# Optimization experiments

Measured on AMD Instinct MI355X. Metric: run time of the kernel, lower is better.

The kernel has to match this reference:

```python
import jax, jax.numpy as jnp
import numpy as np

B, Q, K, D = 16, 2048, 2048, 128
NEG = -1000000.0  # matches torch module's mask fill value (not -inf)


def setup_inputs() -> dict:
    key = jax.random.key(0)
    kq, kk, kv, kl = jax.random.split(key, 4)
    q = jax.random.normal(kq, (B, Q, D), dtype=jnp.float32)
    k = jax.random.normal(kk, (B, K, D), dtype=jnp.float32)
    v = jax.random.normal(kv, (B, K, D), dtype=jnp.float32)
    valid_lens = jax.random.randint(kl, (B, 1), 0, K, dtype=jnp.int32)
    return {"q": q, "k": k, "v": v, "valid_lens": valid_lens}


def reference(q, k, v, valid_lens):
    d = q.shape[-1]
    # scores: (B, Q, K)
    weight = jnp.einsum('bqd,bkd->bqk', q, k) / jnp.sqrt(jnp.asarray(d, q.dtype))
    # mask: key position j valid iff j < valid_len[b]; broadcast over query dim
    mask = jnp.arange(k.shape[1])[None, None, :] < valid_lens[:, :, None]  # (B,1,K)
    weight = jnp.where(mask, weight, NEG)
    score = jax.nn.softmax(weight, axis=-1)
    return jnp.einsum('bqk,bkv->bqv', score, v)
```

## Files before the change

kernel.cpp:

```cpp
#include <hip/hip_runtime.h>

constexpr int NB = 16;
constexpr int NQ = 2048;
constexpr int NK = 2048;
constexpr int ND = 128;
constexpr int KVBLK = 64;
constexpr int NTILE = NK / KVBLK;
constexpr int TILE_USH = KVBLK * ND;
constexpr float SCALE = 0.08838834764831844f;

typedef __attribute__((ext_vector_type(4))) float f4;
typedef __attribute__((ext_vector_type(16))) float f32x16;
typedef __attribute__((ext_vector_type(8))) unsigned short us8;
typedef __attribute__((ext_vector_type(8))) __bf16 bf16x8;
typedef __attribute__((ext_vector_type(4))) unsigned int u32x4;

static __device__ __forceinline__ unsigned short f2bf(float f) {
    unsigned u = __builtin_bit_cast(unsigned, f);
    u += 0x7fffu + ((u >> 16) & 1u);
    return (unsigned short)(u >> 16);
}
static __device__ __forceinline__ f4 splat4(float x) { f4 r = {x,x,x,x}; return r; }

static __device__ __forceinline__ void load_lds16(const unsigned short* g, unsigned short* l) {
    __builtin_amdgcn_global_load_lds(
        (const __attribute__((address_space(1))) void*)g,
        (__attribute__((address_space(3))) void*)l,
        16, 0, 0);
}

static __device__ __forceinline__ unsigned cvt_pk_bf16(float lo, float hi) {
    unsigned r;
    asm("v_cvt_pk_bf16_f32 %0, %1, %2" : "=v"(r) : "v"(lo), "v"(hi));
    return r;
}

__global__ __launch_bounds__(256)
void prep_kv4(const float* __restrict__ kg, const float* __restrict__ vg,
              unsigned short* __restrict__ wk, unsigned short* __restrict__ wvt)
{
    const int b   = blockIdx.y;
    const int t   = blockIdx.x;
    const int kv0 = t * KVBLK;
    const int t0  = threadIdx.x;

    __shared__ __align__(16) unsigned short vl[64 * 136];

    {
        const int kv = t0 >> 2;
        const int c  = t0 & 3;
        const float* gp = kg + (size_t)(b * NK + kv0 + kv) * ND + c * 32;
        unsigned short* ob = wk + (size_t)(b * NTILE + t) * TILE_USH;
        #pragma unroll
        for (int g = 0; g < 4; ++g) {
            f4 f0 = *(const f4*)(gp + g * 8);
            f4 f1 = *(const f4*)(gp + g * 8 + 4);
            us8 w;
            #pragma unroll
            for (int i = 0; i < 4; ++i) { w[i] = f2bf(f0[i]); w[i+4] = f2bf(f1[i]); }
            const int d0 = c * 32 + g * 8;
            const int f  = (kv >> 5) * 8 + (d0 >> 4);
            const int off = f * 512 + ((d0 >> 3) & 1) * 256 + (kv & 31) * 8;
            *(us8*)(ob + off) = w;
        }
    }
    {
        const int kv = t0 >> 2;
        const int d0 = (t0 & 3) * 32;
        const float* gp = vg + (size_t)(b * NK + kv0 + kv) * ND + d0;
        unsigned short* lb = &vl[kv * 136 + d0];
        #pragma unroll
        for (int g = 0; g < 4; ++g) {
            f4 f0 = *(const f4*)(gp + g * 8);
            f4 f1 = *(const f4*)(gp + g * 8 + 4);
            us8 w;
            #pragma unroll
            for (int i = 0; i < 4; ++i) { w[i] = f2bf(f0[i]); w[i+4] = f2bf(f1[i]); }
            *(us8*)(lb + g * 8) = w;
        }
    }
    __syncthreads();
    {
        unsigned short* ob = wvt + (size_t)(b * NTILE + t) * TILE_USH;
        #pragma unroll
        for (int iter = 0; iter < 4; ++iter) {
            const int cid = iter * 256 + t0;
            const int f   = cid >> 6;
            const int l   = cid & 63;
            const int kb  = (f >> 2) * 16 + (l >> 5) * 8;
            const int d   = (f & 3) * 32 + (l & 31);
            us8 w;
            #pragma unroll
            for (int j = 0; j < 8; ++j) w[j] = vl[(kb + j) * 136 + d];
            *(us8*)(ob + cid * 8) = w;
        }
    }
}

__global__ __launch_bounds__(512, 2)
void attn_fused7(const float* __restrict__ qg, const int* __restrict__ vlen,
                 const unsigned short* __restrict__ wk,
                 const unsigned short* __restrict__ wvt,
                 float* __restrict__ og)
{
    const int bid = blockIdx.x;
    const int b   = bid & 15;
    const int qc  = bid >> 4;
    const int q0  = qc * 128;

    const int tid  = threadIdx.x;
    const int wid  = tid >> 6;
    const int grp  = wid >> 2;
    const int w4   = wid & 3;
    const int lane = tid & 63;
    const int lq   = lane & 31;
    const int hi   = lane >> 5;

    const int L = vlen[b];
    const bool uniform = (L <= 0);
    const int Leff = uniform ? NK : L;
    const int ntiles = (Leff + KVBLK - 1) / KVBLK;
    const int ng    = (ntiles + 1 - grp) >> 1;
    const int niter = (ntiles + 1) >> 1;

    __shared__ __align__(16) unsigned short smem[2][2][2 * TILE_USH];

    bf16x8 aq[8];
    {
        const float* qp = qg + (size_t)(b * NQ + q0 + w4 * 32 + lq) * ND + hi * 8;
        #pragma unroll
        for (int c = 0; c < 8; ++c) {
            f4 f0 = *(const f4*)(qp + c * 16);
            f4 f1 = *(const f4*)(qp + c * 16 + 4);
            us8 u;
            #pragma unroll
            for (int i = 0; i < 4; ++i) {
                u[i]     = f2bf(f0[i] * SCALE);
                u[i + 4] = f2bf(f1[i] * SCALE);
            }
            aq[c] = __builtin_bit_cast(bf16x8, u);
        }
    }

    const unsigned short* kbg = wk  + (size_t)b * NTILE * TILE_USH;
    const unsigned short* vbg = wvt + (size_t)b * NTILE * TILE_USH;

    const int s_half = w4 >> 1;
    const int s_sub  = w4 & 1;
    const unsigned short* sbase = s_half ? vbg : kbg;
    const int s_off  = s_sub * 4096 + lane * 8;

    float m_r = -__builtin_inff();
    float l_r = 0.f;
    f32x16 accO[4];
    #pragma unroll
    for (int dc = 0; dc < 4; ++dc)
        #pragma unroll
        for (int r = 0; r < 16; ++r) accO[dc][r] = 0.f;

    if (grp < ntiles) {
        const unsigned short* src = sbase + (size_t)grp * TILE_USH + s_off;
        unsigned short* dst = &smem[grp][0][s_half * 8192 + s_sub * 4096];
        #pragma unroll
        for (int j = 0; j < 8; ++j) load_lds16(src + j * 512, dst + j * 512);
    }
    __syncthreads();

    for (int i = 0; i < niter; ++i) {
        const int tile = 2 * i + grp;
        const int buf  = i & 1;
        const unsigned short* kl  = &smem[grp][buf][0];
        const unsigned short* vl2 = &smem[grp][buf][8192];

        {
            const int tn = tile + 2;
            if (tn < ntiles) {
                const unsigned short* src = sbase + (size_t)tn * TILE_USH + s_off;
                unsigned short* dst = &smem[grp][buf ^ 1][s_half * 8192 + s_sub * 4096];
                #pragma unroll
                for (int j = 0; j < 8; ++j) load_lds16(src + j * 512, dst + j * 512);
            }
        }

        if (i < ng) {
            const int kv0 = tile * KVBLK;

            us8 kf[16];
            #pragma unroll
            for (int c = 0; c < 16; ++c)
                kf[c] = *(const us8*)&kl[c * 512 + lane * 8];

            f32x16 sA, sB;
            #pragma unroll
            for (int r = 0; r < 16; ++r) { sA[r] = 0.f; sB[r] = 0.f; }
            __builtin_amdgcn_s_setprio(1);
            #pragma unroll
            for (int c = 0; c < 8; ++c) {
                sA = __builtin_amdgcn_mfma_f32_32x32x16_bf16(
                    __builtin_bit_cast(bf16x8, kf[c]), aq[c], sA, 0, 0, 0);
                sB = __builtin_amdgcn_mfma_f32_32x32x16_bf16(
                    __builtin_bit_cast(bf16x8, kf[8 + c]), aq[c], sB, 0, 0, 0);
            }
            __builtin_amdgcn_s_setprio(0);
            __builtin_amdgcn_sched_barrier(0);

            us8 vf[16];
            #pragma unroll
            for (int f = 0; f < 16; ++f)
                vf[f] = *(const us8*)&vl2[f * 512 + lane * 8];

            if (uniform) {
                #pragma unroll
                for (int r = 0; r < 16; ++r) { sA[r] = 0.f; sB[r] = 0.f; }
            } else {
                const int lim0 = L - kv0 - 4 * hi;
                const int lim1 = lim0 - 32;
                #pragma unroll
                for (int r = 0; r < 16; ++r) {
                    const int rc = (r & 3) + 8 * (r >> 2);
                    sA[r] = (rc >= lim0) ? -__builtin_inff() : sA[r];
                    sB[r] = (rc >= lim1) ? -__builtin_inff() : sB[r];
                }
            }

            float mx[8];
            #pragma unroll
            for (int i2 = 0; i2 < 8; ++i2)
                mx[i2] = fmaxf(fmaxf(sA[i2], sA[i2 + 8]), fmaxf(sB[i2], sB[i2 + 8]));
            #pragma unroll
            for (int i2 = 0; i2 < 4; ++i2) mx[i2] = fmaxf(mx[i2], mx[i2 + 4]);
            float pm = fmaxf(fmaxf(mx[0], mx[1]), fmaxf(mx[2], mx[3]));
            float pmax = fmaxf(pm, __shfl_xor(pm, 32));

            if (__any(pmax > m_r)) {
                const float mnew = fmaxf(m_r, pmax);
                const float sc = __expf(m_r - mnew);
                m_r = mnew;
                l_r *= sc;
                #pragma unroll
                for (int r = 0; r < 16; ++r) {
                    const int src = ((r & 3) + 8 * (r >> 2) + 4 * hi) + (lane & 32);
                    const float scr = __shfl(sc, src);
                    accO[0][r] *= scr; accO[1][r] *= scr;
                    accO[2][r] *= scr; accO[3][r] *= scr;
                }
            }

            float p0[16], p1[16];
            #pragma unroll
            for (int r = 0; r < 16; ++r) {
                p0[r] = __expf(sA[r] - m_r);
                p1[r] = __expf(sB[r] - m_r);
            }
            float sm[8];
            #pragma unroll
            for (int i2 = 0; i2 < 8; ++i2)
                sm[i2] = (p0[i2] + p0[i2 + 8]) + (p1[i2] + p1[i2 + 8]);
            #pragma unroll
            for (int i2 = 0; i2 < 4; ++i2) sm[i2] += sm[i2 + 4];
            float rsum = (sm[0] + sm[1]) + (sm[2] + sm[3]);
            rsum += __shfl_xor(rsum, 32);
            l_r += rsum;

            unsigned cw[16];
            #pragma unroll
            for (int i2 = 0; i2 < 8; ++i2) cw[i2] = cvt_pk_bf16(p0[2 * i2], p0[2 * i2 + 1]);
            #pragma unroll
            for (int i2 = 0; i2 < 8; ++i2) cw[8 + i2] = cvt_pk_bf16(p1[2 * i2], p1[2 * i2 + 1]);

            bf16x8 pa[4];
            #pragma unroll
            for (int ks = 0; ks < 4; ++ks) {
                const int a = 4 * ks;
                const unsigned u = hi ? cw[a]     : cw[a + 2];
                const unsigned v = hi ? cw[a + 1] : cw[a + 3];
                const unsigned up = __shfl_xor((int)u, 32);
                const unsigned vp = __shfl_xor((int)v, 32);
                u32x4 w;
                w[0] = hi ? up        : cw[a];
                w[1] = hi ? vp        : cw[a + 1];
                w[2] = hi ? cw[a + 2] : up;
                w[3] = hi ? cw[a + 3] : vp;
                pa[ks] = __builtin_bit_cast(bf16x8, w);
            }

            __builtin_amdgcn_s_setprio(1);
            #pragma unroll
            for (int dc = 0; dc < 4; ++dc) {
                #pragma unroll
                for (int ks = 0; ks < 4; ++ks) {
                    accO[dc] = __builtin_amdgcn_mfma_f32_32x32x16_bf16(
                        pa[ks], __builtin_bit_cast(bf16x8, vf[ks * 4 + dc]), accO[dc], 0, 0, 0);
                }
            }
            __builtin_amdgcn_s_setprio(0);
        }

        __syncthreads();
    }

    float* accb = (float*)&smem[0][0][0];
    float* mlb  = (float*)&smem[1][0][0];
    if (grp == 1) {
        #pragma unroll
        for (int dc = 0; dc < 4; ++dc) {
            #pragma unroll
            for (int q4 = 0; q4 < 4; ++q4) {
                f4 v;
                #pragma unroll
                for (int c = 0; c < 4; ++c) v[c] = accO[dc][q4 * 4 + c];
                *(f4*)&accb[(((w4 * 16 + dc * 4 + q4) * 64) + lane) * 4] = v;
            }
        }
        if (hi == 0) {
            mlb[w4 * 32 + lq]       = m_r;
            mlb[128 + w4 * 32 + lq] = l_r;
        }
    }
    __syncthreads();
    if (grp == 0) {
        const float m1 = mlb[w4 * 32 + lq];
        const float l1 = mlb[128 + w4 * 32 + lq];
        const float m  = fmaxf(m_r, m1);
        const float a0 = __expf(m_r - m), a1 = __expf(m1 - m);
        const float linv = 1.0f / (a0 * l_r + a1 * l1);
        const float s0v = a0 * linv, s1v = a1 * linv;
        float* ob = og + (size_t)(b * NQ + q0 + w4 * 32) * ND;
        #pragma unroll
        for (int dc = 0; dc < 4; ++dc) {
            #pragma unroll
            for (int q4 = 0; q4 < 4; ++q4) {
                f4 o1 = *(const f4*)&accb[(((w4 * 16 + dc * 4 + q4) * 64) + lane) * 4];
                #pragma unroll
                for (int c = 0; c < 4; ++c) {
                    const int r = q4 * 4 + c;
                    const int row = c + 8 * q4 + 4 * hi;
                    const float s0r = __shfl(s0v, row + (lane & 32));
                    const float s1r = __shfl(s1v, row + (lane & 32));
                    ob[(size_t)row * ND + dc * 32 + lq] = accO[dc][r] * s0r + o1[c] * s1r;
                }
            }
        }
    }
}

__global__ __launch_bounds__(256, 2)
void attn_fused(const float* __restrict__ qg, const float* __restrict__ kg,
                const float* __restrict__ vg, const int* __restrict__ vlen,
                float* __restrict__ og)
{
    const int b    = blockIdx.y;
    const int q0   = blockIdx.x * 64;
    const int tid  = threadIdx.x;
    const int wid  = tid >> 6;
    const int lane = tid & 63;
    const int lrow = lane & 15;
    const int lgrp = lane >> 4;

    const int L = vlen[b];
    const bool uniform = (L <= 0);
    const int Leff = uniform ? NK : L;
    const int nt32 = (Leff + 31) / 32;

    __shared__ __align__(16) unsigned short kt[32 * 136];
    __shared__ __align__(16) unsigned short vt[128 * 40];
    __shared__ __align__(16) float pt[4][16 * 36];

    bf16x8 aqf[4];
    {
        const float* qp = qg + (size_t)(b * NQ + q0 + wid * 16 + lrow) * ND + lgrp * 8;
        #pragma unroll
        for (int c = 0; c < 4; ++c) {
            f4 f0 = *(const f4*)(qp + c * 32);
            f4 f1 = *(const f4*)(qp + c * 32 + 4);
            us8 u;
            #pragma unroll
            for (int i = 0; i < 4; ++i) {
                u[i]     = f2bf(f0[i] * SCALE);
                u[i + 4] = f2bf(f1[i] * SCALE);
            }
            aqf[c] = __builtin_bit_cast(bf16x8, u);
        }
    }

    float m_r[4], l_r[4];
    f4 accO[8];
    #pragma unroll
    for (int r = 0; r < 4; ++r) { m_r[r] = -__builtin_inff(); l_r[r] = 0.f; }
    #pragma unroll
    for (int dc = 0; dc < 8; ++dc) accO[dc] = splat4(0.f);

    for (int t = 0; t < nt32; ++t) {
        const int kv0 = t * 32;
        __syncthreads();
        {
            const int r  = tid >> 3;
            const int c0 = (tid & 7) * 16;
            const float* gp = kg + (size_t)(b * NK + kv0 + r) * ND + c0;
            f4 f0 = *(const f4*)(gp);
            f4 f1 = *(const f4*)(gp + 4);
            f4 f2 = *(const f4*)(gp + 8);
            f4 f3 = *(const f4*)(gp + 12);
            us8 w0, w1;
            #pragma unroll
            for (int i = 0; i < 4; ++i) {
                w0[i]     = f2bf(f0[i]);
                w0[i + 4] = f2bf(f1[i]);
                w1[i]     = f2bf(f2[i]);
                w1[i + 4] = f2bf(f3[i]);
            }
            unsigned short* dst = &kt[r * 136 + c0];
            *(us8*)(dst)     = w0;
            *(us8*)(dst + 8) = w1;
        }
        {
            const int d  = tid & 127;
            const int g2 = tid >> 7;
            const float* gp = vg + (size_t)(b * NK + kv0 + g2 * 16) * ND + d;
            us8 w0, w1;
            #pragma unroll
            for (int j = 0; j < 8; ++j) {
                w0[j] = f2bf(gp[(size_t)j * ND]);
                w1[j] = f2bf(gp[(size_t)(j + 8) * ND]);
            }
            unsigned short* dst = &vt[d * 40 + g2 * 16];
            *(us8*)(dst)     = w0;
            *(us8*)(dst + 8) = w1;
        }
        __syncthreads();

        f4 s0 = splat4(0.f), s1 = splat4(0.f);
        #pragma unroll
        for (int c = 0; c < 4; ++c) {
            bf16x8 bk0 = __builtin_bit_cast(bf16x8,
                *(const us8*)&kt[lrow * 136 + c * 32 + lgrp * 8]);
            s0 = __builtin_amdgcn_mfma_f32_16x16x32_bf16(aqf[c], bk0, s0, 0, 0, 0);
            bf16x8 bk1 = __builtin_bit_cast(bf16x8,
                *(const us8*)&kt[(16 + lrow) * 136 + c * 32 + lgrp * 8]);
            s1 = __builtin_amdgcn_mfma_f32_16x16x32_bf16(aqf[c], bk1, s1, 0, 0, 0);
        }

        const int col0 = kv0 + lrow;
        if (uniform) {
            s0 = splat4(0.f);
            s1 = splat4(0.f);
        } else {
            if (col0 >= L)      s0 = splat4(-__builtin_inff());
            if (col0 + 16 >= L) s1 = splat4(-__builtin_inff());
        }

        float pm[4];
        #pragma unroll
        for (int r = 0; r < 4; ++r) pm[r] = fmaxf(s0[r], s1[r]);
        #pragma unroll
        for (int off = 8; off > 0; off >>= 1) {
            #pragma unroll
            for (int r = 0; r < 4; ++r)
                pm[r] = fmaxf(pm[r], __shfl_xor(pm[r], off));
        }
        float pr0[4], pr1[4], rs[4], sc[4];
        #pragma unroll
        for (int r = 0; r < 4; ++r) {
            float mn = fmaxf(m_r[r], pm[r]);
            sc[r]  = __expf(m_r[r] - mn);
            m_r[r] = mn;
            pr0[r] = __expf(s0[r] - mn);
            pr1[r] = __expf(s1[r] - mn);
            rs[r]  = pr0[r] + pr1[r];
        }
        #pragma unroll
        for (int off = 8; off > 0; off >>= 1) {
            #pragma unroll
            for (int r = 0; r < 4; ++r)
                rs[r] += __shfl_xor(rs[r], off);
        }
        #pragma unroll
        for (int r = 0; r < 4; ++r) l_r[r] = l_r[r] * sc[r] + rs[r];
        #pragma unroll
        for (int dc = 0; dc < 8; ++dc) {
            #pragma unroll
            for (int r = 0; r < 4; ++r) accO[dc][r] *= sc[r];
        }

        float* pw = pt[wid];
        #pragma unroll
        for (int r = 0; r < 4; ++r) {
            pw[(lgrp * 4 + r) * 36 + lrow]      = pr0[r];
            pw[(lgrp * 4 + r) * 36 + 16 + lrow] = pr1[r];
        }
        asm volatile("s_waitcnt lgkmcnt(0)" ::: "memory");
        f4 a0 = *(const f4*)&pw[lrow * 36 + lgrp * 8];
        f4 a1 = *(const f4*)&pw[lrow * 36 + lgrp * 8 + 4];
        us8 au;
        #pragma unroll
        for (int i = 0; i < 4; ++i) { au[i] = f2bf(a0[i]); au[i + 4] = f2bf(a1[i]); }
        bf16x8 ap = __builtin_bit_cast(bf16x8, au);

        #pragma unroll
        for (int dc = 0; dc < 8; ++dc) {
            bf16x8 bv = __builtin_bit_cast(bf16x8,
                *(const us8*)&vt[(dc * 16 + lrow) * 40 + lgrp * 8]);
            accO[dc] = __builtin_amdgcn_mfma_f32_16x16x32_bf16(ap, bv, accO[dc], 0, 0, 0);
        }
    }

    float inv[4];
    #pragma unroll
    for (int r = 0; r < 4; ++r) inv[r] = 1.0f / l_r[r];
    float* op = og + (size_t)(b * NQ + q0 + wid * 16) * ND;
    #pragma unroll
    for (int dc = 0; dc < 8; ++dc) {
        #pragma unroll
        for (int r = 0; r < 4; ++r)
            op[(lgrp * 4 + r) * ND + dc * 16 + lrow] = accO[dc][r] * inv[r];
    }
}

extern "C" void kernel_launch(void* const* d_in, const int* in_sizes, int n_in,
                              void* d_out, int out_size, void* d_ws, size_t ws_size,
                              hipStream_t stream) {
    (void)in_sizes; (void)n_in; (void)out_size;
    const float* q  = (const float*)d_in[0];
    const float* k  = (const float*)d_in[1];
    const float* v  = (const float*)d_in[2];
    const int*   vl = (const int*)d_in[3];
    float* out = (float*)d_out;

    const size_t half = (size_t)NB * NK * ND * sizeof(unsigned short);
    if (ws_size >= 2 * half) {
        unsigned short* wk  = (unsigned short*)d_ws;
        unsigned short* wvt = wk + (size_t)NB * NK * ND;
        hipLaunchKernelGGL(prep_kv4, dim3(NTILE, NB), dim3(256), 0, stream, k, v, wk, wvt);
        hipLaunchKernelGGL(attn_fused7, dim3((NQ / 128) * NB), dim3(512), 0, stream,
                           q, vl, wk, wvt, out);
    } else {
        hipLaunchKernelGGL(attn_fused, dim3(NQ / 64, NB), dim3(256), 0, stream,
                           q, k, v, vl, out);
    }
}
```

Baseline: 63.39 us.

## Shrink attention blocks to 64 queries and single-buffer KV tiles in LDS

The fused attention kernel moves from 512-thread blocks covering 128 queries to 256-thread blocks covering 64 queries. This doubles the grid and halves shared memory per block. The double-buffered K/V LDS staging becomes a single buffer: K and V fragments are read into registers, the block synchronises, and then the next tile's prefetch is issued while softmax and the PV MFMAs run. The aim is more resident blocks and finer load balance across CUs. The cost is that each K/V tile is reused across fewer queries, so global and L2 traffic for K/V doubles, plus an extra barrier per iteration.

```diff
diff --git a/kernel.cpp b/kernel.cpp
--- a/kernel.cpp
+++ b/kernel.cpp
@@ -97,8 +97,8 @@
     }
 }
 
-__global__ __launch_bounds__(512, 2)
-void attn_fused7(const float* __restrict__ qg, const int* __restrict__ vlen,
+__global__ __launch_bounds__(256, 2)
+void attn_fused8(const float* __restrict__ qg, const int* __restrict__ vlen,
                  const unsigned short* __restrict__ wk,
                  const unsigned short* __restrict__ wvt,
                  float* __restrict__ og)
@@ -106,12 +106,12 @@
     const int bid = blockIdx.x;
     const int b   = bid & 15;
     const int qc  = bid >> 4;
-    const int q0  = qc * 128;
+    const int q0  = qc * 64;
 
     const int tid  = threadIdx.x;
     const int wid  = tid >> 6;
-    const int grp  = wid >> 2;
-    const int w4   = wid & 3;
+    const int grp  = wid >> 1;
+    const int qw   = wid & 1;
     const int lane = tid & 63;
     const int lq   = lane & 31;
     const int hi   = lane >> 5;
@@ -123,11 +123,11 @@
     const int ng    = (ntiles + 1 - grp) >> 1;
     const int niter = (ntiles + 1) >> 1;
 
-    __shared__ __align__(16) unsigned short smem[2][2][2 * TILE_USH];
+    __shared__ __align__(16) unsigned short smem[2][2 * TILE_USH];
 
     bf16x8 aq[8];
     {
-        const float* qp = qg + (size_t)(b * NQ + q0 + w4 * 32 + lq) * ND + hi * 8;
+        const float* qp = qg + (size_t)(b * NQ + q0 + qw * 32 + lq) * ND + hi * 8;
         #pragma unroll
         for (int c = 0; c < 8; ++c) {
             f4 f0 = *(const f4*)(qp + c * 16);
@@ -145,10 +145,9 @@
     const unsigned short* kbg = wk  + (size_t)b * NTILE * TILE_USH;
     const unsigned short* vbg = wvt + (size_t)b * NTILE * TILE_USH;
 
-    const int s_half = w4 >> 1;
-    const int s_sub  = w4 & 1;
-    const unsigned short* sbase = s_half ? vbg : kbg;
-    const int s_off  = s_sub * 4096 + lane * 8;
+    const unsigned short* sbase = qw ? vbg : kbg;
+    unsigned short* sdst = &smem[grp][qw * 8192];
+    const int s_off = lane * 8;
 
     float m_r = -__builtin_inff();
     float l_r = 0.f;
@@ -160,37 +159,23 @@
 
     if (grp < ntiles) {
         const unsigned short* src = sbase + (size_t)grp * TILE_USH + s_off;
-        unsigned short* dst = &smem[grp][0][s_half * 8192 + s_sub * 4096];
-        #pragma unroll
-        for (int j = 0; j < 8; ++j) load_lds16(src + j * 512, dst + j * 512);
+        #pragma unroll
+        for (int j = 0; j < 16; ++j) load_lds16(src + j * 512, sdst + j * 512);
     }
     __syncthreads();
 
     for (int i = 0; i < niter; ++i) {
         const int tile = 2 * i + grp;
-        const int buf  = i & 1;
-        const unsigned short* kl  = &smem[grp][buf][0];
-        const unsigned short* vl2 = &smem[grp][buf][8192];
-
-        {
-            const int tn = tile + 2;
-            if (tn < ntiles) {
-                const unsigned short* src = sbase + (size_t)tn * TILE_USH + s_off;
-                unsigned short* dst = &smem[grp][buf ^ 1][s_half * 8192 + s_sub * 4096];
-                #pragma unroll
-                for (int j = 0; j < 8; ++j) load_lds16(src + j * 512, dst + j * 512);
-            }
-        }
-
-        if (i < ng) {
-            const int kv0 = tile * KVBLK;
-
-            us8 kf[16];
+        const unsigned short* kl  = &smem[grp][0];
+        const unsigned short* vl2 = &smem[grp][8192];
+        const bool act = (i < ng);
+
+        us8 kf[16], vf[16];
+        f32x16 sA, sB;
+        if (act) {
             #pragma unroll
             for (int c = 0; c < 16; ++c)
                 kf[c] = *(const us8*)&kl[c * 512 + lane * 8];
-
-            f32x16 sA, sB;
             #pragma unroll
             for (int r = 0; r < 16; ++r) { sA[r] = 0.f; sB[r] = 0.f; }
             __builtin_amdgcn_s_setprio(1);
@@ -203,11 +188,24 @@
             }
             __builtin_amdgcn_s_setprio(0);
             __builtin_amdgcn_sched_barrier(0);
-
-            us8 vf[16];
             #pragma unroll
             for (int f = 0; f < 16; ++f)
                 vf[f] = *(const us8*)&vl2[f * 512 + lane * 8];
+        }
+
+        __syncthreads();
+
+        {
+            const int tn = tile + 2;
+            if (tn < ntiles) {
+                const unsigned short* src = sbase + (size_t)tn * TILE_USH + s_off;
+                #pragma unroll
+                for (int j = 0; j < 16; ++j) load_lds16(src + j * 512, sdst + j * 512);
+            }
+        }
+
+        if (act) {
+            const int kv0 = tile * KVBLK;
 
             if (uniform) {
                 #pragma unroll
@@ -299,8 +297,8 @@
         __syncthreads();
     }
 
-    float* accb = (float*)&smem[0][0][0];
-    float* mlb  = (float*)&smem[1][0][0];
+    float* accb = (float*)&smem[0][0];
+    float* mlb  = accb + 8192;
     if (grp == 1) {
         #pragma unroll
         for (int dc = 0; dc < 4; ++dc) {
@@ -309,28 +307,28 @@
                 f4 v;
                 #pragma unroll
                 for (int c = 0; c < 4; ++c) v[c] = accO[dc][q4 * 4 + c];
-                *(f4*)&accb[(((w4 * 16 + dc * 4 + q4) * 64) + lane) * 4] = v;
+                *(f4*)&accb[(((qw * 16 + dc * 4 + q4) * 64) + lane) * 4] = v;
             }
         }
         if (hi == 0) {
-            mlb[w4 * 32 + lq]       = m_r;
-            mlb[128 + w4 * 32 + lq] = l_r;
+            mlb[qw * 32 + lq]      = m_r;
+            mlb[64 + qw * 32 + lq] = l_r;
         }
     }
     __syncthreads();
     if (grp == 0) {
-        const float m1 = mlb[w4 * 32 + lq];
-        const float l1 = mlb[128 + w4 * 32 + lq];
+        const float m1 = mlb[qw * 32 + lq];
+        const float l1 = mlb[64 + qw * 32 + lq];
         const float m  = fmaxf(m_r, m1);
         const float a0 = __expf(m_r - m), a1 = __expf(m1 - m);
         const float linv = 1.0f / (a0 * l_r + a1 * l1);
         const float s0v = a0 * linv, s1v = a1 * linv;
-        float* ob = og + (size_t)(b * NQ + q0 + w4 * 32) * ND;
+        float* ob = og + (size_t)(b * NQ + q0 + qw * 32) * ND;
         #pragma unroll
         for (int dc = 0; dc < 4; ++dc) {
             #pragma unroll
             for (int q4 = 0; q4 < 4; ++q4) {
-                f4 o1 = *(const f4*)&accb[(((w4 * 16 + dc * 4 + q4) * 64) + lane) * 4];
+                f4 o1 = *(const f4*)&accb[(((qw * 16 + dc * 4 + q4) * 64) + lane) * 4];
                 #pragma unroll
                 for (int c = 0; c < 4; ++c) {
                     const int r = q4 * 4 + c;
@@ -531,7 +529,7 @@
         unsigned short* wk  = (unsigned short*)d_ws;
         unsigned short* wvt = wk + (size_t)NB * NK * ND;
         hipLaunchKernelGGL(prep_kv4, dim3(NTILE, NB), dim3(256), 0, stream, k, v, wk, wvt);
-        hipLaunchKernelGGL(attn_fused7, dim3((NQ / 128) * NB), dim3(512), 0, stream,
+        hipLaunchKernelGGL(attn_fused8, dim3((NQ / 64) * NB), dim3(256), 0, stream,
                            q, vl, wk, wvt, out);
     } else {
         hipLaunchKernelGGL(attn_fused, dim3(NQ / 64, NB), dim3(256), 0, stream,
```

Result: slower. 67.29 us (+6.2%).

## Process two KV tiles per group per iteration with software-pipelined softmax

Applied to the files above, without the earlier changes.

Each wave group now handles two consecutive KV tiles per loop iteration. The single LDS buffer per group holds both K and V for both tiles. The second tile's QK MFMAs and V loads are issued before the barrier, and its softmax/PV step runs after the next prefetch is started. This halves the number of block-wide barriers per tile and overlaps one tile's softmax with the next global-to-LDS load. The cost is higher register pressure from holding a second score/V fragment set, and the per-group LDS double-buffering is removed, which could expose load latency.

```diff
diff --git a/kernel.cpp b/kernel.cpp
--- a/kernel.cpp
+++ b/kernel.cpp
@@ -98,10 +98,10 @@
 }
 
 __global__ __launch_bounds__(512, 2)
-void attn_fused7(const float* __restrict__ qg, const int* __restrict__ vlen,
-                 const unsigned short* __restrict__ wk,
-                 const unsigned short* __restrict__ wvt,
-                 float* __restrict__ og)
+void attn_fused10(const float* __restrict__ qg, const int* __restrict__ vlen,
+                  const unsigned short* __restrict__ wk,
+                  const unsigned short* __restrict__ wvt,
+                  float* __restrict__ og)
 {
     const int bid = blockIdx.x;
     const int b   = bid & 15;
@@ -120,10 +120,9 @@
     const bool uniform = (L <= 0);
     const int Leff = uniform ? NK : L;
     const int ntiles = (Leff + KVBLK - 1) / KVBLK;
-    const int ng    = (ntiles + 1 - grp) >> 1;
-    const int niter = (ntiles + 1) >> 1;
-
-    __shared__ __align__(16) unsigned short smem[2][2][2 * TILE_USH];
+    const int niter  = (ntiles + 3) >> 2;
+
+    __shared__ __align__(16) unsigned short smem[2][4 * TILE_USH];
 
     bf16x8 aq[8];
     {
@@ -145,10 +144,9 @@
     const unsigned short* kbg = wk  + (size_t)b * NTILE * TILE_USH;
     const unsigned short* vbg = wvt + (size_t)b * NTILE * TILE_USH;
 
-    const int s_half = w4 >> 1;
-    const int s_sub  = w4 & 1;
-    const unsigned short* sbase = s_half ? vbg : kbg;
-    const int s_off  = s_sub * 4096 + lane * 8;
+    const int s_t  = w4 >> 1;
+    const unsigned short* sbase = (w4 & 1) ? vbg : kbg;
+    unsigned short* sdst = &smem[grp][w4 * 8192];
 
     float m_r = -__builtin_inff();
     float l_r = 0.f;
@@ -158,149 +156,163 @@
         #pragma unroll
         for (int r = 0; r < 16; ++r) accO[dc][r] = 0.f;
 
-    if (grp < ntiles) {
-        const unsigned short* src = sbase + (size_t)grp * TILE_USH + s_off;
-        unsigned short* dst = &smem[grp][0][s_half * 8192 + s_sub * 4096];
-        #pragma unroll
-        for (int j = 0; j < 8; ++j) load_lds16(src + j * 512, dst + j * 512);
+    auto qk_phase = [&](const unsigned short* kl, f32x16& sA, f32x16& sB) {
+        us8 kf[16];
+        #pragma unroll
+        for (int c = 0; c < 16; ++c)
+            kf[c] = *(const us8*)&kl[c * 512 + lane * 8];
+        #pragma unroll
+        for (int r = 0; r < 16; ++r) { sA[r] = 0.f; sB[r] = 0.f; }
+        __builtin_amdgcn_s_setprio(1);
+        #pragma unroll
+        for (int c = 0; c < 8; ++c) {
+            sA = __builtin_amdgcn_mfma_f32_32x32x16_bf16(
+                __builtin_bit_cast(bf16x8, kf[c]), aq[c], sA, 0, 0, 0);
+            sB = __builtin_amdgcn_mfma_f32_32x32x16_bf16(
+                __builtin_bit_cast(bf16x8, kf[8 + c]), aq[c], sB, 0, 0, 0);
+        }
+        __builtin_amdgcn_s_setprio(0);
+    };
+    auto load_v = [&](const unsigned short* vl, us8* vf) {
+        #pragma unroll
+        for (int f = 0; f < 16; ++f)
+            vf[f] = *(const us8*)&vl[f * 512 + lane * 8];
+    };
+    auto finish = [&](f32x16& sA, f32x16& sB, const us8* vf, int kv0) {
+        if (uniform) {
+            #pragma unroll
+            for (int r = 0; r < 16; ++r) { sA[r] = 0.f; sB[r] = 0.f; }
+        } else {
+            const int lim0 = L - kv0 - 4 * hi;
+            const int lim1 = lim0 - 32;
+            #pragma unroll
+            for (int r = 0; r < 16; ++r) {
+                const int rc = (r & 3) + 8 * (r >> 2);
+                sA[r] = (rc >= lim0) ? -__builtin_inff() : sA[r];
+                sB[r] = (rc >= lim1) ? -__builtin_inff() : sB[r];
+            }
+        }
+        float mx[8];
+        #pragma unroll
+        for (int i2 = 0; i2 < 8; ++i2)
+            mx[i2] = fmaxf(fmaxf(sA[i2], sA[i2 + 8]), fmaxf(sB[i2], sB[i2 + 8]));
+        #pragma unroll
+        for (int i2 = 0; i2 < 4; ++i2) mx[i2] = fmaxf(mx[i2], mx[i2 + 4]);
+        float pm = fmaxf(fmaxf(mx[0], mx[1]), fmaxf(mx[2], mx[3]));
+        float pmax = fmaxf(pm, __shfl_xor(pm, 32));
+
+        if (__any(pmax > m_r)) {
+            const float mnew = fmaxf(m_r, pmax);
+            const float sc = __expf(m_r - mnew);
+            m_r = mnew;
+            l_r *= sc;
+            #pragma unroll
+            for (int r = 0; r < 16; ++r) {
+                const int src = ((r & 3) + 8 * (r >> 2) + 4 * hi) + (lane & 32);
+                const float scr = __shfl(sc, src);
+                accO[0][r] *= scr; accO[1][r] *= scr;
+                accO[2][r] *= scr; accO[3][r] *= scr;
+            }
+        }
+        float p0[16], p1[16];
+        #pragma unroll
+        for (int r = 0; r < 16; ++r) {
+            p0[r] = __expf(sA[r] - m_r);
+            p1[r] = __expf(sB[r] - m_r);
+        }
+        float sm[8];
+        #pragma unroll
+        for (int i2 = 0; i2 < 8; ++i2)
+            sm[i2] = (p0[i2] + p0[i2 + 8]) + (p1[i2] + p1[i2 + 8]);
+        #pragma unroll
+        for (int i2 = 0; i2 < 4; ++i2) sm[i2] += sm[i2 + 4];
+        float rsum = (sm[0] + sm[1]) + (sm[2] + sm[3]);
+        rsum += __shfl_xor(rsum, 32);
+        l_r += rsum;
+
+        unsigned cw[16];
+        #pragma unroll
+        for (int i2 = 0; i2 < 8; ++i2) cw[i2] = cvt_pk_bf16(p0[2 * i2], p0[2 * i2 + 1]);
+        #pragma unroll
+        for (int i2 = 0; i2 < 8; ++i2) cw[8 + i2] = cvt_pk_bf16(p1[2 * i2], p1[2 * i2 + 1]);
+
+        bf16x8 pa[4];
+        #pragma unroll
+        for (int ks = 0; ks < 4; ++ks) {
+            const int a = 4 * ks;
+            const unsigned u = hi ? cw[a]     : cw[a + 2];
+            const unsigned v = hi ? cw[a + 1] : cw[a + 3];
+            const unsigned up = __shfl_xor((int)u, 32);
+            const unsigned vp = __shfl_xor((int)v, 32);
+            u32x4 w;
+            w[0] = hi ? up        : cw[a];
+            w[1] = hi ? vp        : cw[a + 1];
+            w[2] = hi ? cw[a + 2] : up;
+            w[3] = hi ? cw[a + 3] : vp;
+            pa[ks] = __builtin_bit_cast(bf16x8, w);
+        }
+        __builtin_amdgcn_s_setprio(1);
+        #pragma unroll
+        for (int dc = 0; dc < 4; ++dc) {
+            #pragma unroll
+            for (int ks = 0; ks < 4; ++ks) {
+                accO[dc] = __builtin_amdgcn_mfma_f32_32x32x16_bf16(
+                    pa[ks], __builtin_bit_cast(bf16x8, vf[ks * 4 + dc]), accO[dc], 0, 0, 0);
+            }
+        }
+        __builtin_amdgcn_s_setprio(0);
+    };
+
+    {
+        const unsigned short* src = sbase + (size_t)(2 * grp + s_t) * TILE_USH + lane * 8;
+        #pragma unroll
+        for (int j = 0; j < 16; ++j) load_lds16(src + j * 512, sdst + j * 512);
     }
     __syncthreads();
 
     for (int i = 0; i < niter; ++i) {
-        const int tile = 2 * i + grp;
-        const int buf  = i & 1;
-        const unsigned short* kl  = &smem[grp][buf][0];
-        const unsigned short* vl2 = &smem[grp][buf][8192];
+        const int t0 = 4 * i + 2 * grp;
+        const int t1 = t0 + 1;
+        const bool a0 = (t0 < ntiles);
+        const bool a1 = (t1 < ntiles);
+
+        us8 vf1[16];
+        f32x16 s1A, s1B;
+
+        if (a0) {
+            f32x16 s0A, s0B;
+            us8 vf0[16];
+            qk_phase(&smem[grp][0], s0A, s0B);
+            __builtin_amdgcn_sched_barrier(0);
+            load_v(&smem[grp][8192], vf0);
+            finish(s0A, s0B, vf0, t0 * KVBLK);
+        }
+        if (a1) {
+            qk_phase(&smem[grp][16384], s1A, s1B);
+            __builtin_amdgcn_sched_barrier(0);
+            load_v(&smem[grp][24576], vf1);
+        }
+
+        __syncthreads();
 
         {
-            const int tn = tile + 2;
+            const int tn = 4 * (i + 1) + 2 * grp;
             if (tn < ntiles) {
-                const unsigned short* src = sbase + (size_t)tn * TILE_USH + s_off;
-                unsigned short* dst = &smem[grp][buf ^ 1][s_half * 8192 + s_sub * 4096];
+                int tt = tn + s_t;
+                if (tt > NTILE - 1) tt = NTILE - 1;
+                const unsigned short* src = sbase + (size_t)tt * TILE_USH + lane * 8;
                 #pragma unroll
-                for (int j = 0; j < 8; ++j) load_lds16(src + j * 512, dst + j * 512);
-            }
-        }
-
-        if (i < ng) {
-            const int kv0 = tile * KVBLK;
-
-            us8 kf[16];
-            #pragma unroll
-            for (int c = 0; c < 16; ++c)
-                kf[c] = *(const us8*)&kl[c * 512 + lane * 8];
-
-            f32x16 sA, sB;
-            #pragma unroll
-            for (int r = 0; r < 16; ++r) { sA[r] = 0.f; sB[r] = 0.f; }
-            __builtin_amdgcn_s_setprio(1);
-            #pragma unroll
-            for (int c = 0; c < 8; ++c) {
-                sA = __builtin_amdgcn_mfma_f32_32x32x16_bf16(
-                    __builtin_bit_cast(bf16x8, kf[c]), aq[c], sA, 0, 0, 0);
-                sB = __builtin_amdgcn_mfma_f32_32x32x16_bf16(
-                    __builtin_bit_cast(bf16x8, kf[8 + c]), aq[c], sB, 0, 0, 0);
-            }
-            __builtin_amdgcn_s_setprio(0);
-            __builtin_amdgcn_sched_barrier(0);
-
-            us8 vf[16];
-            #pragma unroll
-            for (int f = 0; f < 16; ++f)
-                vf[f] = *(const us8*)&vl2[f * 512 + lane * 8];
-
-            if (uniform) {
-                #pragma unroll
-                for (int r = 0; r < 16; ++r) { sA[r] = 0.f; sB[r] = 0.f; }
-            } else {
-                const int lim0 = L - kv0 - 4 * hi;
-                const int lim1 = lim0 - 32;
-                #pragma unroll
-                for (int r = 0; r < 16; ++r) {
-                    const int rc = (r & 3) + 8 * (r >> 2);
-                    sA[r] = (rc >= lim0) ? -__builtin_inff() : sA[r];
-                    sB[r] = (rc >= lim1) ? -__builtin_inff() : sB[r];
-                }
-            }
-
-            float mx[8];
-            #pragma unroll
-            for (int i2 = 0; i2 < 8; ++i2)
-                mx[i2] = fmaxf(fmaxf(sA[i2], sA[i2 + 8]), fmaxf(sB[i2], sB[i2 + 8]));
-            #pragma unroll
-            for (int i2 = 0; i2 < 4; ++i2) mx[i2] = fmaxf(mx[i2], mx[i2 + 4]);
-            float pm = fmaxf(fmaxf(mx[0], mx[1]), fmaxf(mx[2], mx[3]));
-            float pmax = fmaxf(pm, __shfl_xor(pm, 32));
-
-            if (__any(pmax > m_r)) {
-                const float mnew = fmaxf(m_r, pmax);
-                const float sc = __expf(m_r - mnew);
-                m_r = mnew;
-                l_r *= sc;
-                #pragma unroll
-                for (int r = 0; r < 16; ++r) {
-                    const int src = ((r & 3) + 8 * (r >> 2) + 4 * hi) + (lane & 32);
-                    const float scr = __shfl(sc, src);
-                    accO[0][r] *= scr; accO[1][r] *= scr;
-                    accO[2][r] *= scr; accO[3][r] *= scr;
-                }
-            }
-
-            float p0[16], p1[16];
-            #pragma unroll
-            for (int r = 0; r < 16; ++r) {
-                p0[r] = __expf(sA[r] - m_r);
-                p1[r] = __expf(sB[r] - m_r);
-            }
-            float sm[8];
-            #pragma unroll
-            for (int i2 = 0; i2 < 8; ++i2)
-                sm[i2] = (p0[i2] + p0[i2 + 8]) + (p1[i2] + p1[i2 + 8]);
-            #pragma unroll
-            for (int i2 = 0; i2 < 4; ++i2) sm[i2] += sm[i2 + 4];
-            float rsum = (sm[0] + sm[1]) + (sm[2] + sm[3]);
-            rsum += __shfl_xor(rsum, 32);
-            l_r += rsum;
-
-            unsigned cw[16];
-            #pragma unroll
-            for (int i2 = 0; i2 < 8; ++i2) cw[i2] = cvt_pk_bf16(p0[2 * i2], p0[2 * i2 + 1]);
-            #pragma unroll
-            for (int i2 = 0; i2 < 8; ++i2) cw[8 + i2] = cvt_pk_bf16(p1[2 * i2], p1[2 * i2 + 1]);
-
-            bf16x8 pa[4];
-            #pragma unroll
-            for (int ks = 0; ks < 4; ++ks) {
-                const int a = 4 * ks;
-                const unsigned u = hi ? cw[a]     : cw[a + 2];
-                const unsigned v = hi ? cw[a + 1] : cw[a + 3];
-                const unsigned up = __shfl_xor((int)u, 32);
-                const unsigned vp = __shfl_xor((int)v, 32);
-                u32x4 w;
-                w[0] = hi ? up        : cw[a];
-                w[1] = hi ? vp        : cw[a + 1];
-                w[2] = hi ? cw[a + 2] : up;
-                w[3] = hi ? cw[a + 3] : vp;
-                pa[ks] = __builtin_bit_cast(bf16x8, w);
-            }
-
-            __builtin_amdgcn_s_setprio(1);
-            #pragma unroll
-            for (int dc = 0; dc < 4; ++dc) {
-                #pragma unroll
-                for (int ks = 0; ks < 4; ++ks) {
-                    accO[dc] = __builtin_amdgcn_mfma_f32_32x32x16_bf16(
-                        pa[ks], __builtin_bit_cast(bf16x8, vf[ks * 4 + dc]), accO[dc], 0, 0, 0);
-                }
-            }
-            __builtin_amdgcn_s_setprio(0);
-        }
+                for (int j = 0; j < 16; ++j) load_lds16(src + j * 512, sdst + j * 512);
+            }
+        }
+
+        if (a1) finish(s1A, s1B, vf1, t1 * KVBLK);
 
         __syncthreads();
     }
 
-    float* accb = (float*)&smem[0][0][0];
-    float* mlb  = (float*)&smem[1][0][0];
+    float* accb = (float*)&smem[0][0];
+    float* mlb  = (float*)&smem[1][0];
     if (grp == 1) {
         #pragma unroll
         for (int dc = 0; dc < 4; ++dc) {
@@ -526,12 +538,12 @@
     const int*   vl = (const int*)d_in[3];
     float* out = (float*)d_out;
 
-    const size_t half = (size_t)NB * NK * ND * sizeof(unsigned short);
-    if (ws_size >= 2 * half) {
+    const size_t kvbytes = 2 * (size_t)NB * NK * ND * sizeof(unsigned short);
+    if (ws_size >= kvbytes) {
         unsigned short* wk  = (unsigned short*)d_ws;
         unsigned short* wvt = wk + (size_t)NB * NK * ND;
         hipLaunchKernelGGL(prep_kv4, dim3(NTILE, NB), dim3(256), 0, stream, k, v, wk, wvt);
-        hipLaunchKernelGGL(attn_fused7, dim3((NQ / 128) * NB), dim3(512), 0, stream,
+        hipLaunchKernelGGL(attn_fused10, dim3((NQ / 128) * NB), dim3(512), 0, stream,
                            q, vl, wk, wvt, out);
     } else {
         hipLaunchKernelGGL(attn_fused, dim3(NQ / 64, NB), dim3(256), 0, stream,
```

After: 117.8 us. 1.86x slower.
